# Kernel optimization log

Hardware: AMD Instinct MI355X
Metric: run time of the kernel (lower is better)

## Reference

```python
import jax, jax.numpy as jnp
import numpy as np

D_MODEL = 256
D_HEAD = 64
N_HEAD = 8


def setup_inputs() -> dict:
    key = jax.random.key(0)
    ks = jax.random.split(key, 8)
    b, h, w = 32, 64, 64
    dk = D_HEAD * N_HEAD
    s = 1.0 / np.sqrt(D_MODEL)
    x = jax.random.normal(ks[0], (b, D_MODEL, h, w), dtype=jnp.float32)
    query = jax.random.normal(ks[1], (b, D_MODEL), dtype=jnp.float32)
    Wkv = jax.random.uniform(ks[2], (2 * dk, D_MODEL), jnp.float32, -s, s)
    bkv = jax.random.uniform(ks[3], (2 * dk,), jnp.float32, -s, s)
    Wq = jax.random.uniform(ks[4], (dk, D_MODEL), jnp.float32, -s, s)
    bq = jax.random.uniform(ks[5], (dk,), jnp.float32, -s, s)
    sf = 1.0 / np.sqrt(dk)
    Wfc = jax.random.uniform(ks[6], (D_MODEL, dk), jnp.float32, -sf, sf)
    bfc = jax.random.uniform(ks[7], (D_MODEL,), jnp.float32, -sf, sf)
    return {"x": x, "query": query, "Wkv": Wkv, "bkv": bkv, "Wq": Wq, "bq": bq, "Wfc": Wfc, "bfc": bfc}


def reference(x, query, Wkv, bkv, Wq, bq, Wfc, bfc):
    b, c, h, w = x.shape
    t = h * w
    scale = 1.0 / np.sqrt(D_HEAD).astype(np.float32)
    # 1x1 conv == per-pixel linear: (b, 2*n*d, t)
    kv = jnp.einsum('bchw,oc->bohw', x, Wkv).reshape(b, 2 * N_HEAD, D_HEAD, t)
    kv = kv + bkv.reshape(1, 2 * N_HEAD, D_HEAD, 1)
    k, v = kv[:, :N_HEAD], kv[:, N_HEAD:]  # each (b, n, d, t)
    q = (query @ Wq.T + bq).reshape(b, N_HEAD, D_HEAD)
    logits = jnp.einsum('bnd,bndj->bnj', q, k) * scale
    attn = jax.nn.softmax(logits, axis=2)
    out = jnp.einsum('bnj,bndj->bnd', attn, v).reshape(b, N_HEAD * D_HEAD)
    return jax.nn.relu(out @ Wfc.T + bfc)
```

## Files before the change

### kernel.cpp

```cpp
#include <hip/hip_runtime.h>
#include <hip/hip_bf16.h>

#define B_     32
#define C_     256
#define T_     4096
#define NH_    8
#define DH_    64

__global__ __launch_bounds__(256) void k_prep(
    const float* __restrict__ query, const float* __restrict__ Wkv,
    const float* __restrict__ bkv, const float* __restrict__ Wq,
    const float* __restrict__ bq, float* __restrict__ qWt,
    float* __restrict__ qb) {
  const int n = blockIdx.x;
  const int b = blockIdx.y;
  const int t = threadIdx.x;
  __shared__ float qrow_s[C_];
  __shared__ float psum[4 * 64];
  __shared__ float qsh[64];
  __shared__ float pb_s[64];

  qrow_s[t] = query[(size_t)b * C_ + t];
  __syncthreads();

  {
    const int d = t & 63, ch = t >> 6;
    const float* wrow = Wq + (size_t)(n * DH_ + d) * C_ + ch * 64;
    const float* qr = qrow_s + ch * 64;
    float s = 0.f;
    #pragma unroll
    for (int c = 0; c < 64; c += 4) {
      float4 w = *(const float4*)(wrow + c);
      s += w.x * qr[c] + w.y * qr[c + 1] + w.z * qr[c + 2] + w.w * qr[c + 3];
    }
    psum[ch * 64 + d] = s;
  }
  __syncthreads();
  if (t < 64)
    qsh[t] = bq[n * DH_ + t] + psum[t] + psum[64 + t] + psum[128 + t] + psum[192 + t];
  __syncthreads();

  const float scale = 0.125f;
  {
    const float* wk = Wkv + (size_t)(n * DH_) * C_ + t;
    float acc = 0.f;
    #pragma unroll 8
    for (int dd = 0; dd < DH_; ++dd) acc += qsh[dd] * wk[(size_t)dd * C_];
    qWt[((size_t)b * C_ + t) * NH_ + n] = acc * scale;
  }
  if (t < 64) pb_s[t] = qsh[t] * bkv[n * DH_ + t];
  __syncthreads();
  if (t == 0) {
    float s = 0.f;
    #pragma unroll 8
    for (int dd = 0; dd < 64; ++dd) s += pb_s[dd];
    qb[b * NH_ + n] = s * scale;
  }
}

__global__ __launch_bounds__(512) void k_logits(
    const float* __restrict__ x, const float* __restrict__ qWt,
    const float* __restrict__ qbv, float* __restrict__ lgraw,
    float* __restrict__ stats) {
  const int jt = blockIdx.x;
  const int b  = blockIdx.y;
  const int t  = threadIdx.x;
  const int tj = t & 255;
  const int th = t >> 8;
  __shared__ float qws[C_ * NH_];
  __shared__ float red[256 * 16];
  __shared__ float sred[8][4];
  __shared__ float ssum[8][4];
  __shared__ float Msh[8];

  {
    const float4 v = *(const float4*)(qWt + (size_t)b * (C_ * NH_) + t * 4);
    *(float4*)(qws + t * 4) = v;
  }
  __syncthreads();

  const int j = jt * 512 + tj * 2;
  const float* xb = x + ((size_t)b * C_ + th * 128) * T_ + j;
  const float* qb = qbv + b * NH_;

  float acc0[NH_], acc1[NH_];
  #pragma unroll
  for (int n = 0; n < NH_; ++n) {
    const float init = (th == 0) ? qb[n] : 0.f;
    acc0[n] = init; acc1[n] = init;
  }

  for (int c0 = 0; c0 < 128; c0 += 16) {
    float2 xv[16];
    #pragma unroll
    for (int cc = 0; cc < 16; ++cc)
      xv[cc] = *(const float2*)(xb + (size_t)(c0 + cc) * T_);
    #pragma unroll
    for (int cc = 0; cc < 16; ++cc) {
      const float4 w0 = *(const float4*)(qws + (th * 128 + c0 + cc) * 8);
      const float4 w1 = *(const float4*)(qws + (th * 128 + c0 + cc) * 8 + 4);
      acc0[0] += w0.x * xv[cc].x; acc1[0] += w0.x * xv[cc].y;
      acc0[1] += w0.y * xv[cc].x; acc1[1] += w0.y * xv[cc].y;
      acc0[2] += w0.z * xv[cc].x; acc1[2] += w0.z * xv[cc].y;
      acc0[3] += w0.w * xv[cc].x; acc1[3] += w0.w * xv[cc].y;
      acc0[4] += w1.x * xv[cc].x; acc1[4] += w1.x * xv[cc].y;
      acc0[5] += w1.y * xv[cc].x; acc1[5] += w1.y * xv[cc].y;
      acc0[6] += w1.z * xv[cc].x; acc1[6] += w1.z * xv[cc].y;
      acc0[7] += w1.w * xv[cc].x; acc1[7] += w1.w * xv[cc].y;
    }
  }

  if (th == 1) {
    float* r = red + tj * 16;
    #pragma unroll
    for (int n = 0; n < NH_; ++n) { r[n] = acc0[n]; r[8 + n] = acc1[n]; }
  }
  __syncthreads();
  if (th == 0) {
    const float* r = red + tj * 16;
    #pragma unroll
    for (int n = 0; n < NH_; ++n) { acc0[n] += r[n]; acc1[n] += r[8 + n]; }
    float* lg = lgraw + ((size_t)b * NH_) * T_ + j;
    #pragma unroll
    for (int n = 0; n < NH_; ++n) {
      float2 o; o.x = acc0[n]; o.y = acc1[n];
      *(float2*)(lg + (size_t)n * T_) = o;
    }
  }

  #pragma unroll
  for (int n = 0; n < NH_; ++n) {
    float mv = fmaxf(acc0[n], acc1[n]);
    #pragma unroll
    for (int o = 32; o >= 1; o >>= 1) mv = fmaxf(mv, __shfl_xor(mv, o));
    if (th == 0 && (tj & 63) == 0) sred[n][tj >> 6] = mv;
  }
  __syncthreads();
  if (t < 8)
    Msh[t] = fmaxf(fmaxf(sred[t][0], sred[t][1]), fmaxf(sred[t][2], sred[t][3]));
  __syncthreads();
  #pragma unroll
  for (int n = 0; n < NH_; ++n) {
    float sv = (th == 0) ? (expf(acc0[n] - Msh[n]) + expf(acc1[n] - Msh[n])) : 0.f;
    #pragma unroll
    for (int o = 32; o >= 1; o >>= 1) sv += __shfl_xor(sv, o);
    if (th == 0 && (tj & 63) == 0) ssum[n][tj >> 6] = sv;
  }
  __syncthreads();
  if (t < 8) {
    const float S = ssum[t][0] + ssum[t][1] + ssum[t][2] + ssum[t][3];
    float2 o; o.x = Msh[t]; o.y = S;
    *(float2*)(stats + ((size_t)(b * NH_ + t) * 8 + jt) * 2) = o;
  }
}

#define BJ_  128
#define BJS_ 32
#define XPITCH_ 33
__global__ __launch_bounds__(256) void k_xattn(
    const float* __restrict__ x, const float* __restrict__ lgraw,
    const float* __restrict__ stats, float* __restrict__ part) {
  const int jt = blockIdx.x;
  const int b  = blockIdx.y;
  const int j0 = jt * BJ_;
  const int t  = threadIdx.x;
  __shared__ float xs[C_ * XPITCH_];
  __shared__ float a_lds[NH_][BJS_];
  __shared__ float Msh[NH_];
  __shared__ float Sish[NH_];

  if (t < NH_) {
    const float* st = stats + (size_t)(b * NH_ + t) * 8 * 2;
    float M = -3.4e38f;
    #pragma unroll
    for (int k = 0; k < 8; ++k) M = fmaxf(M, st[k * 2]);
    float S = 0.f;
    #pragma unroll
    for (int k = 0; k < 8; ++k) S += st[k * 2 + 1] * expf(st[k * 2] - M);
    Msh[t] = M; Sish[t] = 1.0f / S;
  }

  const float* xb  = x + (size_t)b * C_ * T_;
  const float* lgb = lgraw + (size_t)b * NH_ * T_ + j0;

  float acc[NH_];
  #pragma unroll
  for (int n = 0; n < NH_; ++n) acc[n] = 0.f;

  const int cr = t >> 3;
  const int jc = (t & 7) * 4;
  const int an = t >> 5;
  const int aj = t & 31;

  for (int sIt = 0; sIt < BJ_ / BJS_; ++sIt) {
    const int js = sIt * BJS_;
    __syncthreads();
    #pragma unroll
    for (int p = 0; p < 8; ++p) {
      const int c = cr + p * 32;
      float4 vv = *(const float4*)(xb + (size_t)c * T_ + j0 + js + jc);
      float* dst = &xs[c * XPITCH_ + jc];
      dst[0] = vv.x; dst[1] = vv.y; dst[2] = vv.z; dst[3] = vv.w;
    }
    {
      const float lv = lgb[(size_t)an * T_ + js + aj];
      a_lds[an][aj] = expf(lv - Msh[an]) * Sish[an];
    }
    __syncthreads();
    const float* xr = &xs[t * XPITCH_];
    #pragma unroll 4
    for (int jj = 0; jj < BJS_; ++jj) {
      const float xv = xr[jj];
      #pragma unroll
      for (int n = 0; n < NH_; ++n)
        acc[n] += a_lds[n][jj] * xv;
    }
  }

  float* pb = part + ((size_t)b * 32 + jt) * (NH_ * C_);
  #pragma unroll
  for (int n = 0; n < NH_; ++n) pb[n * C_ + t] = acc[n];
}

__global__ __launch_bounds__(256) void k_out2(
    const float* __restrict__ part, const float* __restrict__ Wkv,
    const float* __restrict__ bkv, float* __restrict__ outvG) {
  const int n = blockIdx.x;
  const int b = blockIdx.y;
  const int t = threadIdx.x;
  __shared__ float xa[C_];
  __shared__ float psum[4][64];

  {
    const float* pb = part + (size_t)b * 32 * (NH_ * C_) + n * C_ + t;
    float s = 0.f;
    #pragma unroll
    for (int jt = 0; jt < 32; ++jt) s += pb[(size_t)jt * (NH_ * C_)];
    xa[t] = s;
  }
  __syncthreads();

  {
    const int d = t & 63, q = t >> 6;
    const float* wrow = Wkv + (size_t)(512 + n * 64 + d) * C_ + q * 64;
    const float* xq = xa + q * 64;
    float s = 0.f;
    #pragma unroll
    for (int c = 0; c < 64; c += 4) {
      float4 w = *(const float4*)(wrow + c);
      s += w.x * xq[c] + w.y * xq[c + 1] + w.z * xq[c + 2] + w.w * xq[c + 3];
    }
    psum[q][d] = s;
  }
  __syncthreads();
  if (t < 64)
    outvG[(size_t)b * 512 + n * 64 + t] =
        bkv[512 + n * 64 + t] + psum[0][t] + psum[1][t] + psum[2][t] + psum[3][t];
}

__global__ __launch_bounds__(256) void k_fc(
    const float* __restrict__ outvG, const float* __restrict__ Wfc,
    const float* __restrict__ bfc, float* __restrict__ out) {
  __shared__ float ov[512];
  const int b = blockIdx.x;
  const int t = threadIdx.x;
  ov[t] = outvG[(size_t)b * 512 + t];
  ov[256 + t] = outvG[(size_t)b * 512 + 256 + t];
  __syncthreads();

  const float* wrow = Wfc + (size_t)t * 512;
  float s = bfc[t];
  #pragma unroll 8
  for (int o = 0; o < 512; o += 4) {
    float4 w = *(const float4*)(wrow + o);
    s += w.x * ov[o] + w.y * ov[o + 1] + w.z * ov[o + 2] + w.w * ov[o + 3];
  }
  out[(size_t)b * 256 + t] = fmaxf(s, 0.f);
}

extern "C" void kernel_launch(void* const* d_in, const int* in_sizes, int n_in,
                              void* d_out, int out_size, void* d_ws, size_t ws_size,
                              hipStream_t stream) {
  const float* x     = (const float*)d_in[0];
  const float* query = (const float*)d_in[1];
  const float* Wkv   = (const float*)d_in[2];
  const float* bkv   = (const float*)d_in[3];
  const float* Wq    = (const float*)d_in[4];
  const float* bq    = (const float*)d_in[5];
  const float* Wfc   = (const float*)d_in[6];
  const float* bfc   = (const float*)d_in[7];
  float* out = (float*)d_out;
  float* ws  = (float*)d_ws;

  float* qWt   = ws;
  float* qb    = ws + 65536;
  float* stats = ws + 66048;
  float* lgraw = ws + 70144;
  float* part  = ws + 1118720;
  float* outvG = ws + 3215872;

  k_prep   <<<dim3(NH_, B_), 256, 0, stream>>>(query, Wkv, bkv, Wq, bq, qWt, qb);
  k_logits <<<dim3(8, B_),   512, 0, stream>>>(x, qWt, qb, lgraw, stats);
  k_xattn  <<<dim3(32, B_),  256, 0, stream>>>(x, lgraw, stats, part);
  k_out2   <<<dim3(NH_, B_), 256, 0, stream>>>(part, Wkv, bkv, outvG);
  k_fc     <<<B_,            256, 0, stream>>>(outvG, Wfc, bfc, out);
}
```

Before: 259.6 us.

## Fuse query prep, logits and attention-weighted x into one kernel

Merges the five-kernel pipeline into two. The main kernel computes the projected query, the logits for a 512-pixel tile, and local softmax exponentials. It keeps those exponentials in shared memory and immediately accumulates the weighted sum of x for the same tile, rescaling later in a tail kernel via flash-style max/sum stats. This removes the logits round trip to global memory and the second x read from a cold tile. The price is one block per tile redoing the query projection, and heavy shared memory use (xs plus a_w plus red, around 70KB) with only 256 blocks, which limits occupancy.

```diff
diff --git a/kernel.cpp b/kernel.cpp
--- a/kernel.cpp
+++ b/kernel.cpp
@@ -7,86 +7,76 @@
 #define NH_    8
 #define DH_    64
 
-__global__ __launch_bounds__(256) void k_prep(
-    const float* __restrict__ query, const float* __restrict__ Wkv,
-    const float* __restrict__ bkv, const float* __restrict__ Wq,
-    const float* __restrict__ bq, float* __restrict__ qWt,
-    float* __restrict__ qb) {
-  const int n = blockIdx.x;
-  const int b = blockIdx.y;
-  const int t = threadIdx.x;
-  __shared__ float qrow_s[C_];
-  __shared__ float psum[4 * 64];
-  __shared__ float qsh[64];
-  __shared__ float pb_s[64];
-
-  qrow_s[t] = query[(size_t)b * C_ + t];
-  __syncthreads();
-
-  {
-    const int d = t & 63, ch = t >> 6;
-    const float* wrow = Wq + (size_t)(n * DH_ + d) * C_ + ch * 64;
-    const float* qr = qrow_s + ch * 64;
-    float s = 0.f;
-    #pragma unroll
-    for (int c = 0; c < 64; c += 4) {
-      float4 w = *(const float4*)(wrow + c);
-      s += w.x * qr[c] + w.y * qr[c + 1] + w.z * qr[c + 2] + w.w * qr[c + 3];
-    }
-    psum[ch * 64 + d] = s;
-  }
-  __syncthreads();
-  if (t < 64)
-    qsh[t] = bq[n * DH_ + t] + psum[t] + psum[64 + t] + psum[128 + t] + psum[192 + t];
-  __syncthreads();
-
-  const float scale = 0.125f;
-  {
-    const float* wk = Wkv + (size_t)(n * DH_) * C_ + t;
-    float acc = 0.f;
-    #pragma unroll 8
-    for (int dd = 0; dd < DH_; ++dd) acc += qsh[dd] * wk[(size_t)dd * C_];
-    qWt[((size_t)b * C_ + t) * NH_ + n] = acc * scale;
-  }
-  if (t < 64) pb_s[t] = qsh[t] * bkv[n * DH_ + t];
-  __syncthreads();
-  if (t == 0) {
-    float s = 0.f;
-    #pragma unroll 8
-    for (int dd = 0; dd < 64; ++dd) s += pb_s[dd];
-    qb[b * NH_ + n] = s * scale;
-  }
-}
-
-__global__ __launch_bounds__(512) void k_logits(
-    const float* __restrict__ x, const float* __restrict__ qWt,
-    const float* __restrict__ qbv, float* __restrict__ lgraw,
-    float* __restrict__ stats) {
+#define XP_ 36
+__global__ __launch_bounds__(512) void k_fused(
+    const float* __restrict__ x, const float* __restrict__ query,
+    const float* __restrict__ Wkv, const float* __restrict__ bkv,
+    const float* __restrict__ Wq, const float* __restrict__ bq,
+    float* __restrict__ stats, float* __restrict__ part) {
   const int jt = blockIdx.x;
   const int b  = blockIdx.y;
   const int t  = threadIdx.x;
   const int tj = t & 255;
   const int th = t >> 8;
+
+  __shared__ float qrow_s[C_];
+  __shared__ float q_s[512];
   __shared__ float qws[C_ * NH_];
+  __shared__ float qb_s[NH_];
   __shared__ float red[256 * 16];
   __shared__ float sred[8][4];
   __shared__ float ssum[8][4];
   __shared__ float Msh[8];
-
+  __shared__ __align__(16) float a_w[512][NH_];
+  __shared__ __align__(16) float xs[C_ * XP_];
+
+  if (t < 256) qrow_s[t] = query[(size_t)b * C_ + t];
+  __syncthreads();
   {
-    const float4 v = *(const float4*)(qWt + (size_t)b * (C_ * NH_) + t * 4);
-    *(float4*)(qws + t * 4) = v;
+    const int n = t >> 6, d = t & 63;
+    const float* wrow = Wq + (size_t)(n * DH_ + d) * C_;
+    float s = bq[n * DH_ + d];
+    #pragma unroll
+    for (int c = 0; c < C_; c += 4) {
+      float4 w = *(const float4*)(wrow + c);
+      s += w.x * qrow_s[c] + w.y * qrow_s[c + 1] + w.z * qrow_s[c + 2] + w.w * qrow_s[c + 3];
+    }
+    q_s[t] = s;
+  }
+  __syncthreads();
+  {
+    const float scale = 0.125f;
+    const int c = t & 255, ng = t >> 8;
+    float o4[4];
+    #pragma unroll
+    for (int k = 0; k < 4; ++k) {
+      const int n = ng * 4 + k;
+      const float* wk = Wkv + (size_t)(n * DH_) * C_ + c;
+      const float* qn = q_s + n * DH_;
+      float s = 0.f;
+      #pragma unroll 8
+      for (int d = 0; d < DH_; ++d) s += qn[d] * wk[(size_t)d * C_];
+      o4[k] = s * scale;
+    }
+    *(float4*)&qws[c * 8 + ng * 4] = make_float4(o4[0], o4[1], o4[2], o4[3]);
+  }
+  if (t < NH_) {
+    const float* qn = q_s + t * DH_;
+    const float* bk = bkv + t * DH_;
+    float s = 0.f;
+    #pragma unroll 8
+    for (int d = 0; d < DH_; ++d) s += qn[d] * bk[d];
+    qb_s[t] = s * 0.125f;
   }
   __syncthreads();
 
   const int j = jt * 512 + tj * 2;
   const float* xb = x + ((size_t)b * C_ + th * 128) * T_ + j;
-  const float* qb = qbv + b * NH_;
 
   float acc0[NH_], acc1[NH_];
   #pragma unroll
   for (int n = 0; n < NH_; ++n) {
-    const float init = (th == 0) ? qb[n] : 0.f;
+    const float init = (th == 0) ? qb_s[n] : 0.f;
     acc0[n] = init; acc1[n] = init;
   }
 
@@ -120,12 +110,6 @@
     const float* r = red + tj * 16;
     #pragma unroll
     for (int n = 0; n < NH_; ++n) { acc0[n] += r[n]; acc1[n] += r[8 + n]; }
-    float* lg = lgraw + ((size_t)b * NH_) * T_ + j;
-    #pragma unroll
-    for (int n = 0; n < NH_; ++n) {
-      float2 o; o.x = acc0[n]; o.y = acc1[n];
-      *(float2*)(lg + (size_t)n * T_) = o;
-    }
   }
 
   #pragma unroll
@@ -139,12 +123,24 @@
   if (t < 8)
     Msh[t] = fmaxf(fmaxf(sred[t][0], sred[t][1]), fmaxf(sred[t][2], sred[t][3]));
   __syncthreads();
+  float e0[NH_], e1[NH_];
   #pragma unroll
   for (int n = 0; n < NH_; ++n) {
-    float sv = (th == 0) ? (expf(acc0[n] - Msh[n]) + expf(acc1[n] - Msh[n])) : 0.f;
+    float sv = 0.f;
+    if (th == 0) {
+      e0[n] = expf(acc0[n] - Msh[n]);
+      e1[n] = expf(acc1[n] - Msh[n]);
+      sv = e0[n] + e1[n];
+    }
     #pragma unroll
     for (int o = 32; o >= 1; o >>= 1) sv += __shfl_xor(sv, o);
     if (th == 0 && (tj & 63) == 0) ssum[n][tj >> 6] = sv;
+  }
+  if (th == 0) {
+    *(float4*)&a_w[tj * 2][0]     = make_float4(e0[0], e0[1], e0[2], e0[3]);
+    *(float4*)&a_w[tj * 2][4]     = make_float4(e0[4], e0[5], e0[6], e0[7]);
+    *(float4*)&a_w[tj * 2 + 1][0] = make_float4(e1[0], e1[1], e1[2], e1[3]);
+    *(float4*)&a_w[tj * 2 + 1][4] = make_float4(e1[4], e1[5], e1[6], e1[7]);
   }
   __syncthreads();
   if (t < 8) {
@@ -152,130 +148,125 @@
     float2 o; o.x = Msh[t]; o.y = S;
     *(float2*)(stats + ((size_t)(b * NH_ + t) * 8 + jt) * 2) = o;
   }
+
+  const float* xb2 = x + (size_t)b * C_ * T_ + jt * 512;
+  const int cr  = t >> 3;
+  const int jc  = (t & 7) * 4;
+  const int cc2 = t & 255;
+  const int jh  = t >> 8;
+
+  float acc[NH_];
+  #pragma unroll
+  for (int n = 0; n < NH_; ++n) acc[n] = 0.f;
+
+  for (int sIt = 0; sIt < 16; ++sIt) {
+    const int js = sIt * 32;
+    __syncthreads();
+    #pragma unroll
+    for (int p = 0; p < 4; ++p) {
+      const int c = cr + p * 64;
+      float4 vv = *(const float4*)(xb2 + (size_t)c * T_ + js + jc);
+      *(float4*)&xs[c * XP_ + jc] = vv;
+    }
+    __syncthreads();
+    #pragma unroll
+    for (int g = 0; g < 4; ++g) {
+      const int jj4 = jh * 16 + g * 4;
+      const float4 xv = *(const float4*)&xs[cc2 * XP_ + jj4];
+      #pragma unroll
+      for (int q = 0; q < 4; ++q) {
+        const float4 wlo = *(const float4*)&a_w[js + jj4 + q][0];
+        const float4 whi = *(const float4*)&a_w[js + jj4 + q][4];
+        const float xa = (q == 0) ? xv.x : (q == 1) ? xv.y : (q == 2) ? xv.z : xv.w;
+        acc[0] += wlo.x * xa; acc[1] += wlo.y * xa;
+        acc[2] += wlo.z * xa; acc[3] += wlo.w * xa;
+        acc[4] += whi.x * xa; acc[5] += whi.y * xa;
+        acc[6] += whi.z * xa; acc[7] += whi.w * xa;
+      }
+    }
+  }
+
+  __syncthreads();
+  if (jh == 1) {
+    *(float4*)&red[cc2 * 8]     = make_float4(acc[0], acc[1], acc[2], acc[3]);
+    *(float4*)&red[cc2 * 8 + 4] = make_float4(acc[4], acc[5], acc[6], acc[7]);
+  }
+  __syncthreads();
+  if (jh == 0) {
+    float* pb = part + (((size_t)b * 8 + jt) * NH_) * C_;
+    const float* r = &red[cc2 * 8];
+    #pragma unroll
+    for (int n = 0; n < NH_; ++n)
+      pb[n * C_ + cc2] = acc[n] + r[n];
+  }
 }
 
-#define BJ_  128
-#define BJS_ 32
-#define XPITCH_ 33
-__global__ __launch_bounds__(256) void k_xattn(
-    const float* __restrict__ x, const float* __restrict__ lgraw,
-    const float* __restrict__ stats, float* __restrict__ part) {
-  const int jt = blockIdx.x;
-  const int b  = blockIdx.y;
-  const int j0 = jt * BJ_;
-  const int t  = threadIdx.x;
-  __shared__ float xs[C_ * XPITCH_];
-  __shared__ float a_lds[NH_][BJS_];
-  __shared__ float Msh[NH_];
-  __shared__ float Sish[NH_];
-
-  if (t < NH_) {
-    const float* st = stats + (size_t)(b * NH_ + t) * 8 * 2;
-    float M = -3.4e38f;
-    #pragma unroll
-    for (int k = 0; k < 8; ++k) M = fmaxf(M, st[k * 2]);
-    float S = 0.f;
-    #pragma unroll
-    for (int k = 0; k < 8; ++k) S += st[k * 2 + 1] * expf(st[k * 2] - M);
-    Msh[t] = M; Sish[t] = 1.0f / S;
-  }
-
-  const float* xb  = x + (size_t)b * C_ * T_;
-  const float* lgb = lgraw + (size_t)b * NH_ * T_ + j0;
-
-  float acc[NH_];
-  #pragma unroll
-  for (int n = 0; n < NH_; ++n) acc[n] = 0.f;
-
-  const int cr = t >> 3;
-  const int jc = (t & 7) * 4;
-  const int an = t >> 5;
-  const int aj = t & 31;
-
-  for (int sIt = 0; sIt < BJ_ / BJS_; ++sIt) {
-    const int js = sIt * BJS_;
-    __syncthreads();
-    #pragma unroll
-    for (int p = 0; p < 8; ++p) {
-      const int c = cr + p * 32;
-      float4 vv = *(const float4*)(xb + (size_t)c * T_ + j0 + js + jc);
-      float* dst = &xs[c * XPITCH_ + jc];
-      dst[0] = vv.x; dst[1] = vv.y; dst[2] = vv.z; dst[3] = vv.w;
-    }
-    {
-      const float lv = lgb[(size_t)an * T_ + js + aj];
-      a_lds[an][aj] = expf(lv - Msh[an]) * Sish[an];
-    }
-    __syncthreads();
-    const float* xr = &xs[t * XPITCH_];
-    #pragma unroll 4
-    for (int jj = 0; jj < BJS_; ++jj) {
-      const float xv = xr[jj];
-      #pragma unroll
-      for (int n = 0; n < NH_; ++n)
-        acc[n] += a_lds[n][jj] * xv;
-    }
-  }
-
-  float* pb = part + ((size_t)b * 32 + jt) * (NH_ * C_);
-  #pragma unroll
-  for (int n = 0; n < NH_; ++n) pb[n * C_ + t] = acc[n];
-}
-
-__global__ __launch_bounds__(256) void k_out2(
-    const float* __restrict__ part, const float* __restrict__ Wkv,
-    const float* __restrict__ bkv, float* __restrict__ outvG) {
-  const int n = blockIdx.x;
-  const int b = blockIdx.y;
-  const int t = threadIdx.x;
-  __shared__ float xa[C_];
-  __shared__ float psum[4][64];
-
-  {
-    const float* pb = part + (size_t)b * 32 * (NH_ * C_) + n * C_ + t;
-    float s = 0.f;
-    #pragma unroll
-    for (int jt = 0; jt < 32; ++jt) s += pb[(size_t)jt * (NH_ * C_)];
-    xa[t] = s;
-  }
-  __syncthreads();
-
-  {
-    const int d = t & 63, q = t >> 6;
-    const float* wrow = Wkv + (size_t)(512 + n * 64 + d) * C_ + q * 64;
-    const float* xq = xa + q * 64;
-    float s = 0.f;
-    #pragma unroll
-    for (int c = 0; c < 64; c += 4) {
-      float4 w = *(const float4*)(wrow + c);
-      s += w.x * xq[c] + w.y * xq[c + 1] + w.z * xq[c + 2] + w.w * xq[c + 3];
-    }
-    psum[q][d] = s;
-  }
-  __syncthreads();
-  if (t < 64)
-    outvG[(size_t)b * 512 + n * 64 + t] =
-        bkv[512 + n * 64 + t] + psum[0][t] + psum[1][t] + psum[2][t] + psum[3][t];
-}
-
-__global__ __launch_bounds__(256) void k_fc(
-    const float* __restrict__ outvG, const float* __restrict__ Wfc,
-    const float* __restrict__ bfc, float* __restrict__ out) {
-  __shared__ float ov[512];
+__global__ __launch_bounds__(512) void k_tail(
+    const float* __restrict__ part, const float* __restrict__ stats,
+    const float* __restrict__ Wkv, const float* __restrict__ bkv,
+    const float* __restrict__ Wfc, const float* __restrict__ bfc,
+    float* __restrict__ out) {
   const int b = blockIdx.x;
   const int t = threadIdx.x;
-  ov[t] = outvG[(size_t)b * 512 + t];
-  ov[256 + t] = outvG[(size_t)b * 512 + 256 + t];
-  __syncthreads();
-
-  const float* wrow = Wfc + (size_t)t * 512;
-  float s = bfc[t];
-  #pragma unroll 8
-  for (int o = 0; o < 512; o += 4) {
-    float4 w = *(const float4*)(wrow + o);
-    s += w.x * ov[o] + w.y * ov[o + 1] + w.z * ov[o + 2] + w.w * ov[o + 3];
-  }
-  out[(size_t)b * 256 + t] = fmaxf(s, 0.f);
+  __shared__ float sc[NH_][8];
+  __shared__ float Ml[NH_], Sl[NH_];
+  __shared__ float xa_s[NH_ * C_];
+  __shared__ float ov_s[512];
+
+  if (t < NH_) {
+    const float* st = stats + (size_t)(b * NH_ + t) * 16;
+    float M = -3.4e38f;
+    #pragma unroll
+    for (int k = 0; k < 8; ++k) M = fmaxf(M, st[2 * k]);
+    float S = 0.f;
+    #pragma unroll
+    for (int k = 0; k < 8; ++k) S += st[2 * k + 1] * expf(st[2 * k] - M);
+    Ml[t] = M; Sl[t] = 1.0f / S;
+  }
+  __syncthreads();
+  if (t < 64) {
+    const int n = t >> 3, k = t & 7;
+    const float* st = stats + (size_t)(b * NH_ + n) * 16;
+    sc[n][k] = expf(st[2 * k] - Ml[n]) * Sl[n];
+  }
+  __syncthreads();
+
+  #pragma unroll
+  for (int r = 0; r < 4; ++r) {
+    const int idx = r * 512 + t;
+    const int n = idx >> 8, c = idx & 255;
+    const float* pb = part + ((size_t)b * 8 * NH_) * C_ + n * C_ + c;
+    float s = 0.f;
+    #pragma unroll
+    for (int k = 0; k < 8; ++k) s += sc[n][k] * pb[(size_t)k * NH_ * C_];
+    xa_s[idx] = s;
+  }
+  __syncthreads();
+
+  {
+    const int o = t;
+    const float* wrow = Wkv + (size_t)(512 + o) * C_;
+    const float* xa = &xa_s[(o >> 6) * C_];
+    float s = bkv[512 + o];
+    #pragma unroll 8
+    for (int c = 0; c < C_; c += 4) {
+      float4 w = *(const float4*)(wrow + c);
+      s += w.x * xa[c] + w.y * xa[c + 1] + w.z * xa[c + 2] + w.w * xa[c + 3];
+    }
+    ov_s[o] = s;
+  }
+  __syncthreads();
+
+  if (t < 256) {
+    const float* wrow = Wfc + (size_t)t * 512;
+    float s = bfc[t];
+    #pragma unroll 8
+    for (int o = 0; o < 512; o += 4) {
+      float4 w = *(const float4*)(wrow + o);
+      s += w.x * ov_s[o] + w.y * ov_s[o + 1] + w.z * ov_s[o + 2] + w.w * ov_s[o + 3];
+    }
+    out[(size_t)b * 256 + t] = fmaxf(s, 0.f);
+  }
 }
 
 extern "C" void kernel_launch(void* const* d_in, const int* in_sizes, int n_in,
@@ -292,16 +283,9 @@
   float* out = (float*)d_out;
   float* ws  = (float*)d_ws;
 
-  float* qWt   = ws;
-  float* qb    = ws + 65536;
-  float* stats = ws + 66048;
-  float* lgraw = ws + 70144;
-  float* part  = ws + 1118720;
-  float* outvG = ws + 3215872;
-
-  k_prep   <<<dim3(NH_, B_), 256, 0, stream>>>(query, Wkv, bkv, Wq, bq, qWt, qb);
-  k_logits <<<dim3(8, B_),   512, 0, stream>>>(x, qWt, qb, lgraw, stats);
-  k_xattn  <<<dim3(32, B_),  256, 0, stream>>>(x, lgraw, stats, part);
-  k_out2   <<<dim3(NH_, B_), 256, 0, stream>>>(part, Wkv, bkv, outvG);
-  k_fc     <<<B_,            256, 0, stream>>>(outvG, Wfc, bfc, out);
+  float* stats = ws;
+  float* part  = ws + 4096;
+
+  k_fused<<<dim3(8, B_), 512, 0, stream>>>(x, query, Wkv, bkv, Wq, bq, stats, part);
+  k_tail <<<B_,          512, 0, stream>>>(part, stats, Wkv, bkv, Wfc, bfc, out);
 }
```

After: 293.4 us. 1.13x slower.

## Retile logits kernel for more blocks and fuse output projection kernels

Applied to the files above, without the earlier changes.

The logits kernel now uses 256-thread blocks over 128 columns, 32 blocks per batch instead of 8. Its channel reduction is split four ways and reduced through padded shared memory. The per-block softmax max and sum are now computed within one wavefront, which removes several block barriers, and the stats array widens to 32 partials per head. The out2 and fc kernels are merged into a single 512-thread tail kernel per batch, dropping one launch and the outvG round trip. The trade-off is fewer blocks in the tail stage and more partial stats to combine in xattn.

```diff
diff --git a/kernel.cpp b/kernel.cpp
--- a/kernel.cpp
+++ b/kernel.cpp
@@ -58,47 +58,44 @@
   }
 }
 
-__global__ __launch_bounds__(512) void k_logits(
+__global__ __launch_bounds__(256, 4) void k_logits(
     const float* __restrict__ x, const float* __restrict__ qWt,
     const float* __restrict__ qbv, float* __restrict__ lgraw,
     float* __restrict__ stats) {
   const int jt = blockIdx.x;
   const int b  = blockIdx.y;
   const int t  = threadIdx.x;
-  const int tj = t & 255;
-  const int th = t >> 8;
+  const int tj = t & 63;
+  const int th = t >> 6;
   __shared__ float qws[C_ * NH_];
-  __shared__ float red[256 * 16];
-  __shared__ float sred[8][4];
-  __shared__ float ssum[8][4];
-  __shared__ float Msh[8];
-
-  {
-    const float4 v = *(const float4*)(qWt + (size_t)b * (C_ * NH_) + t * 4);
-    *(float4*)(qws + t * 4) = v;
-  }
-  __syncthreads();
-
-  const int j = jt * 512 + tj * 2;
-  const float* xb = x + ((size_t)b * C_ + th * 128) * T_ + j;
-  const float* qb = qbv + b * NH_;
+  __shared__ float red[4][64][17];
+
+  {
+    const float* src = qWt + (size_t)b * (C_ * NH_);
+    *(float4*)&qws[t * 4] = *(const float4*)(src + t * 4);
+    *(float4*)&qws[1024 + t * 4] = *(const float4*)(src + 1024 + t * 4);
+  }
+  __syncthreads();
+
+  const int j = jt * 128 + tj * 2;
+  const float* xb = x + ((size_t)b * C_ + th * 64) * T_ + j;
 
   float acc0[NH_], acc1[NH_];
   #pragma unroll
   for (int n = 0; n < NH_; ++n) {
-    const float init = (th == 0) ? qb[n] : 0.f;
+    const float init = (th == 0) ? qbv[b * NH_ + n] : 0.f;
     acc0[n] = init; acc1[n] = init;
   }
 
-  for (int c0 = 0; c0 < 128; c0 += 16) {
-    float2 xv[16];
-    #pragma unroll
-    for (int cc = 0; cc < 16; ++cc)
+  for (int c0 = 0; c0 < 64; c0 += 8) {
+    float2 xv[8];
+    #pragma unroll
+    for (int cc = 0; cc < 8; ++cc)
       xv[cc] = *(const float2*)(xb + (size_t)(c0 + cc) * T_);
     #pragma unroll
-    for (int cc = 0; cc < 16; ++cc) {
-      const float4 w0 = *(const float4*)(qws + (th * 128 + c0 + cc) * 8);
-      const float4 w1 = *(const float4*)(qws + (th * 128 + c0 + cc) * 8 + 4);
+    for (int cc = 0; cc < 8; ++cc) {
+      const float4 w0 = *(const float4*)(qws + (th * 64 + c0 + cc) * 8);
+      const float4 w1 = *(const float4*)(qws + (th * 64 + c0 + cc) * 8 + 4);
       acc0[0] += w0.x * xv[cc].x; acc1[0] += w0.x * xv[cc].y;
       acc0[1] += w0.y * xv[cc].x; acc1[1] += w0.y * xv[cc].y;
       acc0[2] += w0.z * xv[cc].x; acc1[2] += w0.z * xv[cc].y;
@@ -110,54 +107,54 @@
     }
   }
 
-  if (th == 1) {
-    float* r = red + tj * 16;
+  if (th != 0) {
+    float* r = &red[th][tj][0];
     #pragma unroll
     for (int n = 0; n < NH_; ++n) { r[n] = acc0[n]; r[8 + n] = acc1[n]; }
   }
   __syncthreads();
   if (th == 0) {
-    const float* r = red + tj * 16;
-    #pragma unroll
-    for (int n = 0; n < NH_; ++n) { acc0[n] += r[n]; acc1[n] += r[8 + n]; }
+    #pragma unroll
+    for (int q = 1; q < 4; ++q) {
+      const float* r = &red[q][tj][0];
+      #pragma unroll
+      for (int n = 0; n < NH_; ++n) { acc0[n] += r[n]; acc1[n] += r[8 + n]; }
+    }
     float* lg = lgraw + ((size_t)b * NH_) * T_ + j;
     #pragma unroll
     for (int n = 0; n < NH_; ++n) {
       float2 o; o.x = acc0[n]; o.y = acc1[n];
       *(float2*)(lg + (size_t)n * T_) = o;
     }
-  }
-
-  #pragma unroll
-  for (int n = 0; n < NH_; ++n) {
-    float mv = fmaxf(acc0[n], acc1[n]);
-    #pragma unroll
-    for (int o = 32; o >= 1; o >>= 1) mv = fmaxf(mv, __shfl_xor(mv, o));
-    if (th == 0 && (tj & 63) == 0) sred[n][tj >> 6] = mv;
-  }
-  __syncthreads();
-  if (t < 8)
-    Msh[t] = fmaxf(fmaxf(sred[t][0], sred[t][1]), fmaxf(sred[t][2], sred[t][3]));
-  __syncthreads();
-  #pragma unroll
-  for (int n = 0; n < NH_; ++n) {
-    float sv = (th == 0) ? (expf(acc0[n] - Msh[n]) + expf(acc1[n] - Msh[n])) : 0.f;
-    #pragma unroll
-    for (int o = 32; o >= 1; o >>= 1) sv += __shfl_xor(sv, o);
-    if (th == 0 && (tj & 63) == 0) ssum[n][tj >> 6] = sv;
-  }
-  __syncthreads();
-  if (t < 8) {
-    const float S = ssum[t][0] + ssum[t][1] + ssum[t][2] + ssum[t][3];
-    float2 o; o.x = Msh[t]; o.y = S;
-    *(float2*)(stats + ((size_t)(b * NH_ + t) * 8 + jt) * 2) = o;
+    float Mv[NH_], Sv[NH_];
+    #pragma unroll
+    for (int n = 0; n < NH_; ++n) {
+      float mv = fmaxf(acc0[n], acc1[n]);
+      #pragma unroll
+      for (int o = 32; o >= 1; o >>= 1) mv = fmaxf(mv, __shfl_xor(mv, o));
+      Mv[n] = mv;
+    }
+    #pragma unroll
+    for (int n = 0; n < NH_; ++n) {
+      float sv = expf(acc0[n] - Mv[n]) + expf(acc1[n] - Mv[n]);
+      #pragma unroll
+      for (int o = 32; o >= 1; o >>= 1) sv += __shfl_xor(sv, o);
+      Sv[n] = sv;
+    }
+    if (tj == 0) {
+      #pragma unroll
+      for (int n = 0; n < NH_; ++n) {
+        float2 o; o.x = Mv[n]; o.y = Sv[n];
+        *(float2*)(stats + ((size_t)(b * NH_ + n) * 32 + jt) * 2) = o;
+      }
+    }
   }
 }
 
 #define BJ_  128
 #define BJS_ 32
 #define XPITCH_ 33
-__global__ __launch_bounds__(256) void k_xattn(
+__global__ __launch_bounds__(256, 4) void k_xattn(
     const float* __restrict__ x, const float* __restrict__ lgraw,
     const float* __restrict__ stats, float* __restrict__ part) {
   const int jt = blockIdx.x;
@@ -170,13 +167,13 @@
   __shared__ float Sish[NH_];
 
   if (t < NH_) {
-    const float* st = stats + (size_t)(b * NH_ + t) * 8 * 2;
+    const float* st = stats + (size_t)(b * NH_ + t) * 64;
     float M = -3.4e38f;
     #pragma unroll
-    for (int k = 0; k < 8; ++k) M = fmaxf(M, st[k * 2]);
+    for (int k = 0; k < 32; ++k) M = fmaxf(M, st[k * 2]);
     float S = 0.f;
     #pragma unroll
-    for (int k = 0; k < 8; ++k) S += st[k * 2 + 1] * expf(st[k * 2] - M);
+    for (int k = 0; k < 32; ++k) S += st[k * 2 + 1] * expf(st[k * 2] - M);
     Msh[t] = M; Sish[t] = 1.0f / S;
   }
 
@@ -222,60 +219,50 @@
   for (int n = 0; n < NH_; ++n) pb[n * C_ + t] = acc[n];
 }
 
-__global__ __launch_bounds__(256) void k_out2(
+__global__ __launch_bounds__(512) void k_tail(
     const float* __restrict__ part, const float* __restrict__ Wkv,
-    const float* __restrict__ bkv, float* __restrict__ outvG) {
-  const int n = blockIdx.x;
-  const int b = blockIdx.y;
-  const int t = threadIdx.x;
-  __shared__ float xa[C_];
-  __shared__ float psum[4][64];
-
-  {
-    const float* pb = part + (size_t)b * 32 * (NH_ * C_) + n * C_ + t;
-    float s = 0.f;
-    #pragma unroll
-    for (int jt = 0; jt < 32; ++jt) s += pb[(size_t)jt * (NH_ * C_)];
-    xa[t] = s;
-  }
-  __syncthreads();
-
-  {
-    const int d = t & 63, q = t >> 6;
-    const float* wrow = Wkv + (size_t)(512 + n * 64 + d) * C_ + q * 64;
-    const float* xq = xa + q * 64;
-    float s = 0.f;
-    #pragma unroll
-    for (int c = 0; c < 64; c += 4) {
-      float4 w = *(const float4*)(wrow + c);
-      s += w.x * xq[c] + w.y * xq[c + 1] + w.z * xq[c + 2] + w.w * xq[c + 3];
-    }
-    psum[q][d] = s;
-  }
-  __syncthreads();
-  if (t < 64)
-    outvG[(size_t)b * 512 + n * 64 + t] =
-        bkv[512 + n * 64 + t] + psum[0][t] + psum[1][t] + psum[2][t] + psum[3][t];
-}
-
-__global__ __launch_bounds__(256) void k_fc(
-    const float* __restrict__ outvG, const float* __restrict__ Wfc,
+    const float* __restrict__ bkv, const float* __restrict__ Wfc,
     const float* __restrict__ bfc, float* __restrict__ out) {
-  __shared__ float ov[512];
   const int b = blockIdx.x;
   const int t = threadIdx.x;
-  ov[t] = outvG[(size_t)b * 512 + t];
-  ov[256 + t] = outvG[(size_t)b * 512 + 256 + t];
-  __syncthreads();
-
-  const float* wrow = Wfc + (size_t)t * 512;
-  float s = bfc[t];
-  #pragma unroll 8
-  for (int o = 0; o < 512; o += 4) {
-    float4 w = *(const float4*)(wrow + o);
-    s += w.x * ov[o] + w.y * ov[o + 1] + w.z * ov[o + 2] + w.w * ov[o + 3];
-  }
-  out[(size_t)b * 256 + t] = fmaxf(s, 0.f);
+  __shared__ float xa_s[NH_ * C_];
+  __shared__ float ov_s[512];
+
+  #pragma unroll
+  for (int r = 0; r < 4; ++r) {
+    const int idx = r * 512 + t;
+    const float* pb = part + (size_t)b * 32 * (NH_ * C_) + idx;
+    float s = 0.f;
+    #pragma unroll
+    for (int k = 0; k < 32; ++k) s += pb[(size_t)k * NH_ * C_];
+    xa_s[idx] = s;
+  }
+  __syncthreads();
+
+  {
+    const int o = t;
+    const float* wrow = Wkv + (size_t)(512 + o) * C_;
+    const float* xa = &xa_s[(o >> 6) * C_];
+    float s = bkv[512 + o];
+    #pragma unroll 8
+    for (int c = 0; c < C_; c += 4) {
+      float4 w = *(const float4*)(wrow + c);
+      s += w.x * xa[c] + w.y * xa[c + 1] + w.z * xa[c + 2] + w.w * xa[c + 3];
+    }
+    ov_s[o] = s;
+  }
+  __syncthreads();
+
+  if (t < 256) {
+    const float* wrow = Wfc + (size_t)t * 512;
+    float s = bfc[t];
+    #pragma unroll 8
+    for (int o = 0; o < 512; o += 4) {
+      float4 w = *(const float4*)(wrow + o);
+      s += w.x * ov_s[o] + w.y * ov_s[o + 1] + w.z * ov_s[o + 2] + w.w * ov_s[o + 3];
+    }
+    out[(size_t)b * 256 + t] = fmaxf(s, 0.f);
+  }
 }
 
 extern "C" void kernel_launch(void* const* d_in, const int* in_sizes, int n_in,
@@ -295,13 +282,11 @@
   float* qWt   = ws;
   float* qb    = ws + 65536;
   float* stats = ws + 66048;
-  float* lgraw = ws + 70144;
-  float* part  = ws + 1118720;
-  float* outvG = ws + 3215872;
+  float* lgraw = ws + 82432;
+  float* part  = ws + 1131008;
 
   k_prep   <<<dim3(NH_, B_), 256, 0, stream>>>(query, Wkv, bkv, Wq, bq, qWt, qb);
-  k_logits <<<dim3(8, B_),   512, 0, stream>>>(x, qWt, qb, lgraw, stats);
+  k_logits <<<dim3(32, B_),  256, 0, stream>>>(x, qWt, qb, lgraw, stats);
   k_xattn  <<<dim3(32, B_),  256, 0, stream>>>(x, lgraw, stats, part);
-  k_out2   <<<dim3(NH_, B_), 256, 0, stream>>>(part, Wkv, bkv, outvG);
-  k_fc     <<<B_,            256, 0, stream>>>(outvG, Wfc, bfc, out);
-}
+  k_tail   <<<B_,            512, 0, stream>>>(part, Wkv, bkv, Wfc, bfc, out);
+}
```

Result: slower. 273.5 us (+5.3%).
